# Kernel tuning notes

Hardware: AMD Instinct MI355X
Metric: run time of the kernel (lower is better)

Reference implementation:

```python
import jax, jax.numpy as jnp
import numpy as np

H = 128
N_ATOMS = 20000
N_BONDS = 60000
BATCH = 8


def _linear_params(key, fan_in, fan_out, bias=True):
    kw, kb = jax.random.split(key)
    lim = 1.0 / np.sqrt(fan_in)
    W = jax.random.uniform(kw, (fan_in, fan_out), jnp.float32, -lim, lim)
    if bias:
        b = jax.random.uniform(kb, (fan_out,), jnp.float32, -lim, lim)
        return W, b
    return W


def setup_inputs() -> dict:
    key = jax.random.key(0)
    ks = jax.random.split(key, 12)
    h = jax.random.normal(ks[0], (BATCH, N_ATOMS, H), jnp.float32)
    x = jax.random.normal(ks[1], (BATCH, N_ATOMS, 3), jnp.float32)
    bond_indices = jax.random.randint(ks[2], (N_BONDS, 2), 0, N_ATOMS, jnp.int64)
    Wm1, bm1 = _linear_params(ks[3], 2 * H + 1, H)
    Wm2, bm2 = _linear_params(ks[4], H, H)
    Wn1, bn1 = _linear_params(ks[5], 2 * H, H)
    Wn2, bn2 = _linear_params(ks[6], H, H)
    Wc1, bc1 = _linear_params(ks[7], H, H)
    # xavier_uniform gain=0.001 for final coord layer [1, H] in torch -> [H, 1] here
    lim = 0.001 * np.sqrt(6.0 / (H + 1))
    Wc2 = jax.random.uniform(ks[8], (H, 1), jnp.float32, -lim, lim)
    return dict(h=h, x=x, bond_indices=bond_indices,
                Wm1=Wm1, bm1=bm1, Wm2=Wm2, bm2=bm2,
                Wn1=Wn1, bn1=bn1, Wn2=Wn2, bn2=bn2,
                Wc1=Wc1, bc1=bc1, Wc2=Wc2)


def reference(h, x, bond_indices, Wm1, bm1, Wm2, bm2, Wn1, bn1, Wn2, bn2, Wc1, bc1, Wc2):
    silu = jax.nn.silu
    n_atoms = h.shape[1]
    src = bond_indices[:, 0]
    dst = bond_indices[:, 1]

    h_src = h[:, src, :]            # [B, E, H]
    h_dst = h[:, dst, :]
    coord_diff = x[:, dst, :] - x[:, src, :]   # [B, E, 3]
    dist = jnp.linalg.norm(coord_diff, axis=-1, keepdims=True)  # [B, E, 1]

    mi = jnp.concatenate([h_src, h_dst, dist], axis=-1)  # [B, E, 2H+1]
    messages = silu(silu(mi @ Wm1 + bm1) @ Wm2 + bm2)    # [B, E, H]

    aggregated = jnp.zeros_like(h).at[:, dst, :].add(messages).at[:, src, :].add(messages)

    h_in = jnp.concatenate([h, aggregated], axis=-1)     # [B, N, 2H]
    h_out = h + (silu(h_in @ Wn1 + bn1) @ Wn2 + bn2)

    coord_weights = silu(messages @ Wc1 + bc1) @ Wc2     # [B, E, 1]
    coord_diff_norm = coord_diff / (dist + 1e-8)
    upd = coord_diff_norm * coord_weights                # [B, E, 3]
    coord_update = jnp.zeros_like(x).at[:, dst, :].add(upd).at[:, src, :].add(-upd)

    ones = jnp.ones(src.shape[0], dtype=h.dtype)
    bond_counts = jnp.zeros(n_atoms, dtype=h.dtype).at[dst].add(ones).at[src].add(ones)
    bond_counts = jnp.clip(bond_counts, 1.0, None)
    x_out = x + coord_update / bond_counts[None, :, None]
    return h_out, x_out
```

## Files before the change

### kernel.cpp

```cpp
#include <hip/hip_runtime.h>


#define H      128
#define NA     20000
#define NB     60000
#define NBATCH 8
#define ADJ_CAP 32

typedef __bf16 bf16;
typedef __bf16 bf16x4 __attribute__((ext_vector_type(4)));
typedef __bf16 bf16x8 __attribute__((ext_vector_type(8)));
typedef float  f32x4  __attribute__((ext_vector_type(4)));

__device__ __forceinline__ float silu_f(float v) {
  float e = __expf(-v);
  return v * __builtin_amdgcn_rcpf(1.0f + e);
}

__device__ __forceinline__ int tswz(int row, int col) {
  return (row << 7) + (((((col) >> 3) ^ (row & 7)) << 3) | (col & 7));
}

__global__ void cast_h(const float* __restrict__ src, bf16* __restrict__ dst) {
  int i = blockIdx.x * 256 + threadIdx.x;
  float4 v = *(const float4*)(src + (size_t)i * 4);
  bf16x4 t = {(bf16)v.x, (bf16)v.y, (bf16)v.z, (bf16)v.w};
  *(bf16x4*)(dst + (size_t)i * 4) = t;
}

__global__ void pack_w(const float* __restrict__ src, bf16* __restrict__ dst,
                       int K) {
  int i = blockIdx.x * 256 + threadIdx.x;
  if (i >= K * 128) return;
  int k = i >> 7, n = i & 127;
  int nt = n >> 4, ks = k >> 5;
  int lane = (((k >> 3) & 3) << 4) | (n & 15);
  int j = k & 7;
  int KS = K >> 5;
  dst[((((nt * KS + ks) * 64) + lane) << 3) + j] = (bf16)src[i];
}

__global__ void build_adj2(const int* __restrict__ bonds,
                           int* __restrict__ degI, int* __restrict__ adj2) {
  int e = blockIdx.x * 256 + threadIdx.x;
  if (e >= NB) return;
  int s = bonds[2 * e], d = bonds[2 * e + 1];
  int p = atomicAdd(&degI[s], 1);
  if (p < ADJ_CAP) adj2[s * ADJ_CAP + p] = (e << 1);
  p = atomicAdd(&degI[d], 1);
  if (p < ADJ_CAP) adj2[d * ADJ_CAP + p] = (e << 1) | 1;
}

__global__ __launch_bounds__(256, 6) void msg_kernel(
    const bf16* __restrict__ hb, const float* __restrict__ x,
    const int* __restrict__ bonds,
    const bf16* __restrict__ W1p, const float* __restrict__ bm1,
    const bf16* __restrict__ W2p, const float* __restrict__ bm2,
    const float* __restrict__ w1c,
    const bf16* __restrict__ Wc1p, const float* __restrict__ bc1,
    const float* __restrict__ Wc2,
    bf16* __restrict__ msgOut, float* __restrict__ updv) {
  __shared__ __align__(16) bf16 Tbuf[32 * 128];
  __shared__ float cds[32 * 3];
  __shared__ float dists[32];
  __shared__ float bm1s[128], bm2s[128], w1cs[128], bc1s[128], wc2s[128];
  __shared__ float cwpart[2][32];

  const int tid = threadIdx.x, blk = blockIdx.x;

  if (tid < 32) {
    int Rg = blk * 32 + tid;
    int bond = Rg >> 3, batch = Rg & 7;
    int s = bonds[2 * bond], dn = bonds[2 * bond + 1];
    const float* xs = x + (size_t)(batch * NA + s) * 3;
    const float* xd = x + (size_t)(batch * NA + dn) * 3;
    float c0 = xd[0] - xs[0], c1 = xd[1] - xs[1], c2 = xd[2] - xs[2];
    cds[tid * 3 + 0] = c0; cds[tid * 3 + 1] = c1; cds[tid * 3 + 2] = c2;
    dists[tid] = sqrtf(c0 * c0 + c1 * c1 + c2 * c2);
  }
  if (tid < 128) {
    bm1s[tid] = bm1[tid]; bm2s[tid] = bm2[tid]; w1cs[tid] = w1c[tid];
    bc1s[tid] = bc1[tid]; wc2s[tid] = Wc2[tid];
  }
  __syncthreads();

  const int lane = tid & 63;
  const int quad = lane >> 4, l16 = lane & 15;
  const int wave = tid >> 6;
  const int rowBase = (wave >> 1) * 16;
  const int colG = wave & 1;
  const int colBase = colG * 64;
  const bf16x8* W1v = (const bf16x8*)W1p;
  const bf16x8* W2v = (const bf16x8*)W2p;
  const bf16x8* Wc1v = (const bf16x8*)Wc1p;

  const int RgA = blk * 32 + rowBase + l16;
  const int bondA = RgA >> 3, batA = RgA & 7;
  const bf16* hsrc = hb + (size_t)(batA * NA + bonds[2 * bondA]) * H;
  const bf16* hdst = hb + (size_t)(batA * NA + bonds[2 * bondA + 1]) * H;

  f32x4 acc[4];
#pragma unroll
  for (int nt = 0; nt < 4; nt++) acc[nt] = (f32x4){0.f, 0.f, 0.f, 0.f};

#pragma unroll
  for (int ks = 0; ks < 4; ks++) {
    bf16x8 a = *(const bf16x8*)(hsrc + ks * 32 + quad * 8);
#pragma unroll
    for (int nt = 0; nt < 4; nt++) {
      bf16x8 b = W1v[((colG * 4 + nt) * 8 + ks) * 64 + lane];
      acc[nt] = __builtin_amdgcn_mfma_f32_16x16x32_bf16(a, b, acc[nt], 0, 0, 0);
    }
  }
#pragma unroll
  for (int ks = 4; ks < 8; ks++) {
    bf16x8 a = *(const bf16x8*)(hdst + (ks - 4) * 32 + quad * 8);
#pragma unroll
    for (int nt = 0; nt < 4; nt++) {
      bf16x8 b = W1v[((colG * 4 + nt) * 8 + ks) * 64 + lane];
      acc[nt] = __builtin_amdgcn_mfma_f32_16x16x32_bf16(a, b, acc[nt], 0, 0, 0);
    }
  }
#pragma unroll
  for (int nt = 0; nt < 4; nt++) {
    int col = colBase + nt * 16 + l16;
    float bb = bm1s[col], wc = w1cs[col];
#pragma unroll
    for (int reg = 0; reg < 4; reg++) {
      int row = rowBase + quad * 4 + reg;
      float v = acc[nt][reg] + bb + dists[row] * wc;
      Tbuf[tswz(row, col)] = (bf16)silu_f(v);
    }
  }
  __syncthreads();

#pragma unroll
  for (int nt = 0; nt < 4; nt++) acc[nt] = (f32x4){0.f, 0.f, 0.f, 0.f};
#pragma unroll
  for (int ks = 0; ks < 4; ks++) {
    bf16x8 a = *(const bf16x8*)&Tbuf[tswz(rowBase + l16, ks * 32 + quad * 8)];
#pragma unroll
    for (int nt = 0; nt < 4; nt++) {
      bf16x8 b = W2v[((colG * 4 + nt) * 4 + ks) * 64 + lane];
      acc[nt] = __builtin_amdgcn_mfma_f32_16x16x32_bf16(a, b, acc[nt], 0, 0, 0);
    }
  }
  __syncthreads();
#pragma unroll
  for (int nt = 0; nt < 4; nt++) {
    int col = colBase + nt * 16 + l16;
    float bb = bm2s[col];
#pragma unroll
    for (int reg = 0; reg < 4; reg++) {
      int row = rowBase + quad * 4 + reg;
      Tbuf[tswz(row, col)] = (bf16)silu_f(acc[nt][reg] + bb);
    }
  }
  __syncthreads();

#pragma unroll
  for (int nt = 0; nt < 4; nt++) acc[nt] = (f32x4){0.f, 0.f, 0.f, 0.f};
#pragma unroll
  for (int ks = 0; ks < 4; ks++) {
    bf16x8 a = *(const bf16x8*)&Tbuf[tswz(rowBase + l16, ks * 32 + quad * 8)];
#pragma unroll
    for (int nt = 0; nt < 4; nt++) {
      bf16x8 b = Wc1v[((colG * 4 + nt) * 4 + ks) * 64 + lane];
      acc[nt] = __builtin_amdgcn_mfma_f32_16x16x32_bf16(a, b, acc[nt], 0, 0, 0);
    }
  }

#pragma unroll
  for (int i = 0; i < 2; i++) {
    int item = i * 64 + lane;
    int row = rowBase + (item >> 3);
    int cg = colG * 8 + (item & 7);
    *(bf16x8*)&msgOut[(size_t)(blk * 32 + row) * H + cg * 8] =
        *(const bf16x8*)&Tbuf[tswz(row, cg * 8)];
  }

  float cwp[4] = {0.f, 0.f, 0.f, 0.f};
#pragma unroll
  for (int nt = 0; nt < 4; nt++) {
    int col = colBase + nt * 16 + l16;
    float bb = bc1s[col], w2 = wc2s[col];
#pragma unroll
    for (int reg = 0; reg < 4; reg++)
      cwp[reg] += silu_f(acc[nt][reg] + bb) * w2;
  }
#pragma unroll
  for (int reg = 0; reg < 4; reg++) {
    float s = cwp[reg];
    s += __shfl_xor(s, 1);
    s += __shfl_xor(s, 2);
    s += __shfl_xor(s, 4);
    s += __shfl_xor(s, 8);
    cwp[reg] = s;
  }
  if (l16 == 0) {
#pragma unroll
    for (int reg = 0; reg < 4; reg++)
      cwpart[colG][rowBase + quad * 4 + reg] = cwp[reg];
  }
  __syncthreads();
  if (colG == 0 && l16 == 0) {
#pragma unroll
    for (int reg = 0; reg < 4; reg++) {
      int row = rowBase + quad * 4 + reg;
      size_t Rg = (size_t)blk * 32 + row;
      float cw = cwpart[0][row] + cwpart[1][row];
      float inv = 1.0f / (dists[row] + 1e-8f);
#pragma unroll
      for (int c = 0; c < 3; c++)
        updv[Rg * 3 + c] = cds[row * 3 + c] * inv * cw;
    }
  }
}

__global__ __launch_bounds__(256, 6) void node_kernel(
    const float* __restrict__ h, const bf16* __restrict__ hb,
    const bf16* __restrict__ msg, const float* __restrict__ updv,
    const int* __restrict__ degI, const int* __restrict__ adj2,
    const bf16* __restrict__ Wn1p, const float* __restrict__ bn1,
    const bf16* __restrict__ Wn2p, const float* __restrict__ bn2,
    const float* __restrict__ x,
    float* __restrict__ hout, float* __restrict__ xout) {
  __shared__ __align__(16) bf16 Abuf[32 * 128];
  __shared__ __align__(16) bf16 Tbuf[32 * 128];

  const int tid = threadIdx.x, blk = blockIdx.x;

  {
    const int row = tid >> 3, c8 = tid & 7;
    const int Rg = blk * 32 + row;
    const int atomA = Rg % NA, batA = Rg / NA;
    int deg = degI[atomA];
    if (deg > ADJ_CAP) deg = ADJ_CAP;
    const int* ap = adj2 + atomA * ADJ_CAP;
    float a16[16];
#pragma unroll
    for (int t = 0; t < 16; t++) a16[t] = 0.f;
    float sx = 0.f, sy = 0.f, sz = 0.f;
    int j = 0;
    for (; j + 4 <= deg; j += 4) {
      int4 e4 = *(const int4*)&ap[j];
      const bf16* m0 = msg + ((size_t)(e4.x >> 1) * 8 + batA) * H + c8 * 16;
      const bf16* m1 = msg + ((size_t)(e4.y >> 1) * 8 + batA) * H + c8 * 16;
      const bf16* m2 = msg + ((size_t)(e4.z >> 1) * 8 + batA) * H + c8 * 16;
      const bf16* m3 = msg + ((size_t)(e4.w >> 1) * 8 + batA) * H + c8 * 16;
      bf16x8 v0 = *(const bf16x8*)(m0), v1 = *(const bf16x8*)(m0 + 8);
      bf16x8 u0 = *(const bf16x8*)(m1), u1 = *(const bf16x8*)(m1 + 8);
      bf16x8 p0 = *(const bf16x8*)(m2), p1 = *(const bf16x8*)(m2 + 8);
      bf16x8 q0 = *(const bf16x8*)(m3), q1 = *(const bf16x8*)(m3 + 8);
      if (c8 == 0) {
        float sg0 = (e4.x & 1) ? 1.0f : -1.0f;
        float sg1 = (e4.y & 1) ? 1.0f : -1.0f;
        float sg2 = (e4.z & 1) ? 1.0f : -1.0f;
        float sg3 = (e4.w & 1) ? 1.0f : -1.0f;
        const float* uv0 = updv + ((size_t)(e4.x >> 1) * 8 + batA) * 3;
        const float* uv1 = updv + ((size_t)(e4.y >> 1) * 8 + batA) * 3;
        const float* uv2 = updv + ((size_t)(e4.z >> 1) * 8 + batA) * 3;
        const float* uv3 = updv + ((size_t)(e4.w >> 1) * 8 + batA) * 3;
        sx += sg0 * uv0[0] + sg1 * uv1[0] + sg2 * uv2[0] + sg3 * uv3[0];
        sy += sg0 * uv0[1] + sg1 * uv1[1] + sg2 * uv2[1] + sg3 * uv3[1];
        sz += sg0 * uv0[2] + sg1 * uv1[2] + sg2 * uv2[2] + sg3 * uv3[2];
      }
#pragma unroll
      for (int t = 0; t < 8; t++) {
        a16[t]     += ((float)v0[t] + (float)u0[t]) + ((float)p0[t] + (float)q0[t]);
        a16[8 + t] += ((float)v1[t] + (float)u1[t]) + ((float)p1[t] + (float)q1[t]);
      }
    }
    for (; j < deg; j++) {
      int ent0 = ap[j];
      const bf16* m0 = msg + ((size_t)(ent0 >> 1) * 8 + batA) * H + c8 * 16;
      bf16x8 v0 = *(const bf16x8*)(m0);
      bf16x8 v1 = *(const bf16x8*)(m0 + 8);
      if (c8 == 0) {
        float sg0 = (ent0 & 1) ? 1.0f : -1.0f;
        const float* uv0 = updv + ((size_t)(ent0 >> 1) * 8 + batA) * 3;
        sx += sg0 * uv0[0]; sy += sg0 * uv0[1]; sz += sg0 * uv0[2];
      }
#pragma unroll
      for (int t = 0; t < 8; t++) {
        a16[t]     += (float)v0[t];
        a16[8 + t] += (float)v1[t];
      }
    }
    if (c8 == 0) {
      float cnt = deg < 1 ? 1.0f : (float)deg;
      float inv = 1.0f / cnt;
      size_t o = (size_t)Rg * 3;
      xout[o + 0] = x[o + 0] + sx * inv;
      xout[o + 1] = x[o + 1] + sy * inv;
      xout[o + 2] = x[o + 2] + sz * inv;
    }
    bf16x8 w0, w1;
#pragma unroll
    for (int t = 0; t < 8; t++) { w0[t] = (bf16)a16[t]; w1[t] = (bf16)a16[8 + t]; }
    *(bf16x8*)&Abuf[tswz(row, c8 * 16)]     = w0;
    *(bf16x8*)&Abuf[tswz(row, c8 * 16 + 8)] = w1;
  }
  __syncthreads();

  const int lane = tid & 63, wave = tid >> 6;
  const int quad = lane >> 4, l16 = lane & 15;
  const int rowG = (wave >> 1) * 16, colG = wave & 1, colBase = colG * 64;
  const int RgA = blk * 32 + rowG + l16;
  const bf16* hrow = hb + (size_t)RgA * H;
  const bf16x8* W1v = (const bf16x8*)Wn1p;
  const bf16x8* W2v = (const bf16x8*)Wn2p;

  f32x4 acc[4];
#pragma unroll
  for (int nt = 0; nt < 4; nt++) acc[nt] = (f32x4){0.f, 0.f, 0.f, 0.f};

#pragma unroll
  for (int ks = 0; ks < 4; ks++) {
    bf16x8 a = *(const bf16x8*)(hrow + ks * 32 + quad * 8);
#pragma unroll
    for (int nt = 0; nt < 4; nt++) {
      bf16x8 b = W1v[((colG * 4 + nt) * 8 + ks) * 64 + lane];
      acc[nt] = __builtin_amdgcn_mfma_f32_16x16x32_bf16(a, b, acc[nt], 0, 0, 0);
    }
  }
#pragma unroll
  for (int ks2 = 0; ks2 < 4; ks2++) {
    bf16x8 a = *(const bf16x8*)&Abuf[tswz(rowG + l16, ks2 * 32 + quad * 8)];
#pragma unroll
    for (int nt = 0; nt < 4; nt++) {
      bf16x8 b = W1v[((colG * 4 + nt) * 8 + 4 + ks2) * 64 + lane];
      acc[nt] = __builtin_amdgcn_mfma_f32_16x16x32_bf16(a, b, acc[nt], 0, 0, 0);
    }
  }
#pragma unroll
  for (int nt = 0; nt < 4; nt++) {
    int col = colBase + nt * 16 + l16;
    float bb = bn1[col];
#pragma unroll
    for (int reg = 0; reg < 4; reg++) {
      int row = rowG + quad * 4 + reg;
      Tbuf[tswz(row, col)] = (bf16)silu_f(acc[nt][reg] + bb);
    }
  }
  __syncthreads();

#pragma unroll
  for (int nt = 0; nt < 4; nt++) acc[nt] = (f32x4){0.f, 0.f, 0.f, 0.f};
#pragma unroll
  for (int ks = 0; ks < 4; ks++) {
    bf16x8 a = *(const bf16x8*)&Tbuf[tswz(rowG + l16, ks * 32 + quad * 8)];
#pragma unroll
    for (int nt = 0; nt < 4; nt++) {
      bf16x8 b = W2v[((colG * 4 + nt) * 4 + ks) * 64 + lane];
      acc[nt] = __builtin_amdgcn_mfma_f32_16x16x32_bf16(a, b, acc[nt], 0, 0, 0);
    }
  }
#pragma unroll
  for (int nt = 0; nt < 4; nt++) {
    int col = colBase + nt * 16 + l16;
    float bb = bn2[col];
#pragma unroll
    for (int reg = 0; reg < 4; reg++) {
      size_t Ro = (size_t)blk * 32 + rowG + quad * 4 + reg;
      hout[Ro * H + col] = h[Ro * H + col] + acc[nt][reg] + bb;
    }
  }
}

extern "C" void kernel_launch(void* const* d_in, const int* in_sizes, int n_in,
                              void* d_out, int out_size, void* d_ws,
                              size_t ws_size, hipStream_t stream) {
  const float* h    = (const float*)d_in[0];
  const float* x    = (const float*)d_in[1];
  const int*  bonds = (const int*)d_in[2];
  const float* Wm1  = (const float*)d_in[3];
  const float* bm1  = (const float*)d_in[4];
  const float* Wm2  = (const float*)d_in[5];
  const float* bm2  = (const float*)d_in[6];
  const float* Wn1  = (const float*)d_in[7];
  const float* bn1  = (const float*)d_in[8];
  const float* Wn2  = (const float*)d_in[9];
  const float* bn2  = (const float*)d_in[10];
  const float* Wc1  = (const float*)d_in[11];
  const float* bc1  = (const float*)d_in[12];
  const float* Wc2  = (const float*)d_in[13];

  float* out  = (float*)d_out;
  float* hout = out;
  float* xout = out + (size_t)NBATCH * NA * H;

  char* ws = (char*)d_ws;
  const size_t OFF_DEG  = 0;
  const size_t OFF_W1   = 163840;
  const size_t OFF_W2   = OFF_W1 + 65536;
  const size_t OFF_WN1  = OFF_W2 + 32768;
  const size_t OFF_WN2  = OFF_WN1 + 65536;
  const size_t OFF_WC1  = OFF_WN2 + 32768;
  const size_t OFF_ADJ2 = 393216;
  const size_t OFF_UPDV = 2953216;
  const size_t OFF_HB   = 8713216;
  const size_t OFF_MSG  = 49673216;

  int*   degI = (int*)(ws + OFF_DEG);
  bf16*  W1p  = (bf16*)(ws + OFF_W1);
  bf16*  W2p  = (bf16*)(ws + OFF_W2);
  bf16*  Wn1p = (bf16*)(ws + OFF_WN1);
  bf16*  Wn2p = (bf16*)(ws + OFF_WN2);
  bf16*  Wc1p = (bf16*)(ws + OFF_WC1);
  int*   adj2 = (int*)(ws + OFF_ADJ2);
  float* updv = (float*)(ws + OFF_UPDV);
  bf16*  hb   = (bf16*)(ws + OFF_HB);
  bf16*  msgB = (bf16*)(ws + OFF_MSG);

  (void)hipMemsetAsync(degI, 0, NA * sizeof(int), stream);

  cast_h<<<NBATCH * NA * H / 1024, 256, 0, stream>>>(h, hb);
  pack_w<<<128, 256, 0, stream>>>(Wm1, W1p, 256);
  pack_w<<<64, 256, 0, stream>>>(Wm2, W2p, 128);
  pack_w<<<128, 256, 0, stream>>>(Wn1, Wn1p, 256);
  pack_w<<<64, 256, 0, stream>>>(Wn2, Wn2p, 128);
  pack_w<<<64, 256, 0, stream>>>(Wc1, Wc1p, 128);

  build_adj2<<<(NB + 255) / 256, 256, 0, stream>>>(bonds, degI, adj2);

  msg_kernel<<<NB * NBATCH / 32, 256, 0, stream>>>(
      hb, x, bonds, W1p, bm1, W2p, bm2, Wm1 + 256 * H, Wc1p, bc1, Wc2,
      msgB, updv);
  node_kernel<<<NBATCH * NA / 32, 256, 0, stream>>>(
      h, hb, msgB, updv, degI, adj2, Wn1p, bn1, Wn2p, bn2, x,
      hout, xout);
}
```

Baseline: 509.9 us.

## Double msg_kernel rows per block and prefetch adjacency with null-padded entries

msg_kernel now handles 64 rows per block instead of 32. Each wave computes two 16-row MFMA tiles that share the same weight fragment loads, which halves weight traffic per row and gives more independent MFMAs to overlap. The occupancy hint drops from 6 to 4 blocks per SIMD to make room for the extra registers. Separately, the adjacency list is pre-filled with a null entry that points to a zeroed msg/updv slot. This lets node_kernel load the first eight neighbours unconditionally and start the gathers before reading the degree, at the cost of wasted gathers for low-degree atoms and an extra init kernel.

New measurement: 503.2 us. No clear change (-1.3%).

```diff
diff --git a/kernel.cpp b/kernel.cpp
--- a/kernel.cpp
+++ b/kernel.cpp
@@ -6,6 +6,7 @@
 #define NB     60000
 #define NBATCH 8
 #define ADJ_CAP 32
+#define NULL_ENT (NB << 1)
 
 typedef __bf16 bf16;
 typedef __bf16 bf16x4 __attribute__((ext_vector_type(4)));
@@ -40,6 +41,12 @@
   dst[((((nt * KS + ks) * 64) + lane) << 3) + j] = (bf16)src[i];
 }
 
+__global__ void init_adj(int* __restrict__ degI, int* __restrict__ adj2) {
+  int i = blockIdx.x * 256 + threadIdx.x;
+  if (i < NA) degI[i] = 0;
+  if (i < NA * ADJ_CAP) adj2[i] = NULL_ENT;
+}
+
 __global__ void build_adj2(const int* __restrict__ bonds,
                            int* __restrict__ degI, int* __restrict__ adj2) {
   int e = blockIdx.x * 256 + threadIdx.x;
@@ -51,7 +58,7 @@
   if (p < ADJ_CAP) adj2[d * ADJ_CAP + p] = (e << 1) | 1;
 }
 
-__global__ __launch_bounds__(256, 6) void msg_kernel(
+__global__ __launch_bounds__(256, 4) void msg_kernel(
     const bf16* __restrict__ hb, const float* __restrict__ x,
     const int* __restrict__ bonds,
     const bf16* __restrict__ W1p, const float* __restrict__ bm1,
@@ -60,16 +67,16 @@
     const bf16* __restrict__ Wc1p, const float* __restrict__ bc1,
     const float* __restrict__ Wc2,
     bf16* __restrict__ msgOut, float* __restrict__ updv) {
-  __shared__ __align__(16) bf16 Tbuf[32 * 128];
-  __shared__ float cds[32 * 3];
-  __shared__ float dists[32];
+  __shared__ __align__(16) bf16 Tbuf[64 * 128];
+  __shared__ float cds[64 * 3];
+  __shared__ float dists[64];
   __shared__ float bm1s[128], bm2s[128], w1cs[128], bc1s[128], wc2s[128];
-  __shared__ float cwpart[2][32];
+  __shared__ float cwpart[2][64];
 
   const int tid = threadIdx.x, blk = blockIdx.x;
 
-  if (tid < 32) {
-    int Rg = blk * 32 + tid;
+  if (tid < 64) {
+    int Rg = blk * 64 + tid;
     int bond = Rg >> 3, batch = Rg & 7;
     int s = bonds[2 * bond], dn = bonds[2 * bond + 1];
     const float* xs = x + (size_t)(batch * NA + s) * 3;
@@ -87,38 +94,49 @@
   const int lane = tid & 63;
   const int quad = lane >> 4, l16 = lane & 15;
   const int wave = tid >> 6;
-  const int rowBase = (wave >> 1) * 16;
+  const int rowBase = (wave >> 1) * 32;
   const int colG = wave & 1;
   const int colBase = colG * 64;
   const bf16x8* W1v = (const bf16x8*)W1p;
   const bf16x8* W2v = (const bf16x8*)W2p;
   const bf16x8* Wc1v = (const bf16x8*)Wc1p;
 
-  const int RgA = blk * 32 + rowBase + l16;
-  const int bondA = RgA >> 3, batA = RgA & 7;
-  const bf16* hsrc = hb + (size_t)(batA * NA + bonds[2 * bondA]) * H;
-  const bf16* hdst = hb + (size_t)(batA * NA + bonds[2 * bondA + 1]) * H;
-
-  f32x4 acc[4];
-#pragma unroll
-  for (int nt = 0; nt < 4; nt++) acc[nt] = (f32x4){0.f, 0.f, 0.f, 0.f};
+  const int Rg0 = blk * 64 + rowBase + l16;
+  const int bn0 = Rg0 >> 3, bat0 = Rg0 & 7;
+  const bf16* hs0 = hb + (size_t)(bat0 * NA + bonds[2 * bn0]) * H;
+  const bf16* hd0 = hb + (size_t)(bat0 * NA + bonds[2 * bn0 + 1]) * H;
+  const int Rg1 = Rg0 + 16;
+  const int bn1_ = Rg1 >> 3, bat1 = Rg1 & 7;
+  const bf16* hs1 = hb + (size_t)(bat1 * NA + bonds[2 * bn1_]) * H;
+  const bf16* hd1 = hb + (size_t)(bat1 * NA + bonds[2 * bn1_ + 1]) * H;
+
+  f32x4 acc0[4], acc1[4];
+#pragma unroll
+  for (int nt = 0; nt < 4; nt++) {
+    acc0[nt] = (f32x4){0.f, 0.f, 0.f, 0.f};
+    acc1[nt] = (f32x4){0.f, 0.f, 0.f, 0.f};
+  }
 
 #pragma unroll
   for (int ks = 0; ks < 4; ks++) {
-    bf16x8 a = *(const bf16x8*)(hsrc + ks * 32 + quad * 8);
+    bf16x8 a0 = *(const bf16x8*)(hs0 + ks * 32 + quad * 8);
+    bf16x8 a1 = *(const bf16x8*)(hs1 + ks * 32 + quad * 8);
 #pragma unroll
     for (int nt = 0; nt < 4; nt++) {
       bf16x8 b = W1v[((colG * 4 + nt) * 8 + ks) * 64 + lane];
-      acc[nt] = __builtin_amdgcn_mfma_f32_16x16x32_bf16(a, b, acc[nt], 0, 0, 0);
+      acc0[nt] = __builtin_amdgcn_mfma_f32_16x16x32_bf16(a0, b, acc0[nt], 0, 0, 0);
+      acc1[nt] = __builtin_amdgcn_mfma_f32_16x16x32_bf16(a1, b, acc1[nt], 0, 0, 0);
     }
   }
 #pragma unroll
   for (int ks = 4; ks < 8; ks++) {
-    bf16x8 a = *(const bf16x8*)(hdst + (ks - 4) * 32 + quad * 8);
+    bf16x8 a0 = *(const bf16x8*)(hd0 + (ks - 4) * 32 + quad * 8);
+    bf16x8 a1 = *(const bf16x8*)(hd1 + (ks - 4) * 32 + quad * 8);
 #pragma unroll
     for (int nt = 0; nt < 4; nt++) {
       bf16x8 b = W1v[((colG * 4 + nt) * 8 + ks) * 64 + lane];
-      acc[nt] = __builtin_amdgcn_mfma_f32_16x16x32_bf16(a, b, acc[nt], 0, 0, 0);
+      acc0[nt] = __builtin_amdgcn_mfma_f32_16x16x32_bf16(a0, b, acc0[nt], 0, 0, 0);
+      acc1[nt] = __builtin_amdgcn_mfma_f32_16x16x32_bf16(a1, b, acc1[nt], 0, 0, 0);
     }
   }
 #pragma unroll
@@ -127,22 +145,28 @@
     float bb = bm1s[col], wc = w1cs[col];
 #pragma unroll
     for (int reg = 0; reg < 4; reg++) {
-      int row = rowBase + quad * 4 + reg;
-      float v = acc[nt][reg] + bb + dists[row] * wc;
-      Tbuf[tswz(row, col)] = (bf16)silu_f(v);
-    }
-  }
-  __syncthreads();
-
-#pragma unroll
-  for (int nt = 0; nt < 4; nt++) acc[nt] = (f32x4){0.f, 0.f, 0.f, 0.f};
+      int row0 = rowBase + quad * 4 + reg;
+      int row1 = row0 + 16;
+      Tbuf[tswz(row0, col)] = (bf16)silu_f(acc0[nt][reg] + bb + dists[row0] * wc);
+      Tbuf[tswz(row1, col)] = (bf16)silu_f(acc1[nt][reg] + bb + dists[row1] * wc);
+    }
+  }
+  __syncthreads();
+
+#pragma unroll
+  for (int nt = 0; nt < 4; nt++) {
+    acc0[nt] = (f32x4){0.f, 0.f, 0.f, 0.f};
+    acc1[nt] = (f32x4){0.f, 0.f, 0.f, 0.f};
+  }
 #pragma unroll
   for (int ks = 0; ks < 4; ks++) {
-    bf16x8 a = *(const bf16x8*)&Tbuf[tswz(rowBase + l16, ks * 32 + quad * 8)];
+    bf16x8 a0 = *(const bf16x8*)&Tbuf[tswz(rowBase + l16, ks * 32 + quad * 8)];
+    bf16x8 a1 = *(const bf16x8*)&Tbuf[tswz(rowBase + 16 + l16, ks * 32 + quad * 8)];
 #pragma unroll
     for (int nt = 0; nt < 4; nt++) {
       bf16x8 b = W2v[((colG * 4 + nt) * 4 + ks) * 64 + lane];
-      acc[nt] = __builtin_amdgcn_mfma_f32_16x16x32_bf16(a, b, acc[nt], 0, 0, 0);
+      acc0[nt] = __builtin_amdgcn_mfma_f32_16x16x32_bf16(a0, b, acc0[nt], 0, 0, 0);
+      acc1[nt] = __builtin_amdgcn_mfma_f32_16x16x32_bf16(a1, b, acc1[nt], 0, 0, 0);
     }
   }
   __syncthreads();
@@ -152,67 +176,82 @@
     float bb = bm2s[col];
 #pragma unroll
     for (int reg = 0; reg < 4; reg++) {
-      int row = rowBase + quad * 4 + reg;
-      Tbuf[tswz(row, col)] = (bf16)silu_f(acc[nt][reg] + bb);
-    }
-  }
-  __syncthreads();
-
-#pragma unroll
-  for (int nt = 0; nt < 4; nt++) acc[nt] = (f32x4){0.f, 0.f, 0.f, 0.f};
+      int row0 = rowBase + quad * 4 + reg;
+      int row1 = row0 + 16;
+      Tbuf[tswz(row0, col)] = (bf16)silu_f(acc0[nt][reg] + bb);
+      Tbuf[tswz(row1, col)] = (bf16)silu_f(acc1[nt][reg] + bb);
+    }
+  }
+  __syncthreads();
+
+#pragma unroll
+  for (int nt = 0; nt < 4; nt++) {
+    acc0[nt] = (f32x4){0.f, 0.f, 0.f, 0.f};
+    acc1[nt] = (f32x4){0.f, 0.f, 0.f, 0.f};
+  }
 #pragma unroll
   for (int ks = 0; ks < 4; ks++) {
-    bf16x8 a = *(const bf16x8*)&Tbuf[tswz(rowBase + l16, ks * 32 + quad * 8)];
+    bf16x8 a0 = *(const bf16x8*)&Tbuf[tswz(rowBase + l16, ks * 32 + quad * 8)];
+    bf16x8 a1 = *(const bf16x8*)&Tbuf[tswz(rowBase + 16 + l16, ks * 32 + quad * 8)];
 #pragma unroll
     for (int nt = 0; nt < 4; nt++) {
       bf16x8 b = Wc1v[((colG * 4 + nt) * 4 + ks) * 64 + lane];
-      acc[nt] = __builtin_amdgcn_mfma_f32_16x16x32_bf16(a, b, acc[nt], 0, 0, 0);
-    }
-  }
-
-#pragma unroll
-  for (int i = 0; i < 2; i++) {
-    int item = i * 64 + lane;
-    int row = rowBase + (item >> 3);
-    int cg = colG * 8 + (item & 7);
-    *(bf16x8*)&msgOut[(size_t)(blk * 32 + row) * H + cg * 8] =
+      acc0[nt] = __builtin_amdgcn_mfma_f32_16x16x32_bf16(a0, b, acc0[nt], 0, 0, 0);
+      acc1[nt] = __builtin_amdgcn_mfma_f32_16x16x32_bf16(a1, b, acc1[nt], 0, 0, 0);
+    }
+  }
+
+#pragma unroll
+  for (int i = 0; i < 4; i++) {
+    int item = i * 256 + tid;
+    int row = item >> 4, cg = item & 15;
+    *(bf16x8*)&msgOut[(size_t)(blk * 64 + row) * H + cg * 8] =
         *(const bf16x8*)&Tbuf[tswz(row, cg * 8)];
   }
 
-  float cwp[4] = {0.f, 0.f, 0.f, 0.f};
+  float cwp0[4] = {0.f, 0.f, 0.f, 0.f};
+  float cwp1[4] = {0.f, 0.f, 0.f, 0.f};
 #pragma unroll
   for (int nt = 0; nt < 4; nt++) {
     int col = colBase + nt * 16 + l16;
     float bb = bc1s[col], w2 = wc2s[col];
 #pragma unroll
-    for (int reg = 0; reg < 4; reg++)
-      cwp[reg] += silu_f(acc[nt][reg] + bb) * w2;
+    for (int reg = 0; reg < 4; reg++) {
+      cwp0[reg] += silu_f(acc0[nt][reg] + bb) * w2;
+      cwp1[reg] += silu_f(acc1[nt][reg] + bb) * w2;
+    }
   }
 #pragma unroll
   for (int reg = 0; reg < 4; reg++) {
-    float s = cwp[reg];
-    s += __shfl_xor(s, 1);
-    s += __shfl_xor(s, 2);
-    s += __shfl_xor(s, 4);
-    s += __shfl_xor(s, 8);
-    cwp[reg] = s;
+    float s0 = cwp0[reg], s1 = cwp1[reg];
+    s0 += __shfl_xor(s0, 1); s1 += __shfl_xor(s1, 1);
+    s0 += __shfl_xor(s0, 2); s1 += __shfl_xor(s1, 2);
+    s0 += __shfl_xor(s0, 4); s1 += __shfl_xor(s1, 4);
+    s0 += __shfl_xor(s0, 8); s1 += __shfl_xor(s1, 8);
+    cwp0[reg] = s0; cwp1[reg] = s1;
   }
   if (l16 == 0) {
 #pragma unroll
-    for (int reg = 0; reg < 4; reg++)
-      cwpart[colG][rowBase + quad * 4 + reg] = cwp[reg];
+    for (int reg = 0; reg < 4; reg++) {
+      int row0 = rowBase + quad * 4 + reg;
+      cwpart[colG][row0] = cwp0[reg];
+      cwpart[colG][row0 + 16] = cwp1[reg];
+    }
   }
   __syncthreads();
   if (colG == 0 && l16 == 0) {
 #pragma unroll
     for (int reg = 0; reg < 4; reg++) {
-      int row = rowBase + quad * 4 + reg;
-      size_t Rg = (size_t)blk * 32 + row;
-      float cw = cwpart[0][row] + cwpart[1][row];
-      float inv = 1.0f / (dists[row] + 1e-8f);
-#pragma unroll
-      for (int c = 0; c < 3; c++)
-        updv[Rg * 3 + c] = cds[row * 3 + c] * inv * cw;
+#pragma unroll
+      for (int rs = 0; rs < 2; rs++) {
+        int row = rowBase + quad * 4 + reg + rs * 16;
+        size_t Rg = (size_t)blk * 64 + row;
+        float cw = cwpart[0][row] + cwpart[1][row];
+        float inv = 1.0f / (dists[row] + 1e-8f);
+#pragma unroll
+        for (int c = 0; c < 3; c++)
+          updv[Rg * 3 + c] = cds[row * 3 + c] * inv * cw;
+      }
     }
   }
 }
@@ -234,16 +273,18 @@
     const int row = tid >> 3, c8 = tid & 7;
     const int Rg = blk * 32 + row;
     const int atomA = Rg % NA, batA = Rg / NA;
+    const int* ap = adj2 + atomA * ADJ_CAP;
     int deg = degI[atomA];
+    int4 eA = *(const int4*)&ap[0];
+    int4 eB = *(const int4*)&ap[4];
     if (deg > ADJ_CAP) deg = ADJ_CAP;
-    const int* ap = adj2 + atomA * ADJ_CAP;
+
     float a16[16];
 #pragma unroll
     for (int t = 0; t < 16; t++) a16[t] = 0.f;
     float sx = 0.f, sy = 0.f, sz = 0.f;
-    int j = 0;
-    for (; j + 4 <= deg; j += 4) {
-      int4 e4 = *(const int4*)&ap[j];
+
+    auto gather4 = [&](int4 e4) {
       const bf16* m0 = msg + ((size_t)(e4.x >> 1) * 8 + batA) * H + c8 * 16;
       const bf16* m1 = msg + ((size_t)(e4.y >> 1) * 8 + batA) * H + c8 * 16;
       const bf16* m2 = msg + ((size_t)(e4.z >> 1) * 8 + batA) * H + c8 * 16;
@@ -270,7 +311,12 @@
         a16[t]     += ((float)v0[t] + (float)u0[t]) + ((float)p0[t] + (float)q0[t]);
         a16[8 + t] += ((float)v1[t] + (float)u1[t]) + ((float)p1[t] + (float)q1[t]);
       }
-    }
+    };
+
+    gather4(eA);
+    gather4(eB);
+    int j = 8;
+    for (; j + 4 <= deg; j += 4) gather4(*(const int4*)&ap[j]);
     for (; j < deg; j++) {
       int ent0 = ap[j];
       const bf16* m0 = msg + ((size_t)(ent0 >> 1) * 8 + batA) * H + c8 * 16;
@@ -399,8 +445,8 @@
   const size_t OFF_WC1  = OFF_WN2 + 32768;
   const size_t OFF_ADJ2 = 393216;
   const size_t OFF_UPDV = 2953216;
-  const size_t OFF_HB   = 8713216;
-  const size_t OFF_MSG  = 49673216;
+  const size_t OFF_HB   = 8717312;
+  const size_t OFF_MSG  = 49677312;
 
   int*   degI = (int*)(ws + OFF_DEG);
   bf16*  W1p  = (bf16*)(ws + OFF_W1);
@@ -413,7 +459,10 @@
   bf16*  hb   = (bf16*)(ws + OFF_HB);
   bf16*  msgB = (bf16*)(ws + OFF_MSG);
 
-  (void)hipMemsetAsync(degI, 0, NA * sizeof(int), stream);
+  (void)hipMemsetAsync(msgB + (size_t)NB * 8 * H, 0, 8 * H * sizeof(bf16),
+                       stream);
+  (void)hipMemsetAsync(updv + (size_t)NB * 8 * 3, 0, 8 * 3 * sizeof(float),
+                       stream);
 
   cast_h<<<NBATCH * NA * H / 1024, 256, 0, stream>>>(h, hb);
   pack_w<<<128, 256, 0, stream>>>(Wm1, W1p, 256);
@@ -422,9 +471,10 @@
   pack_w<<<64, 256, 0, stream>>>(Wn2, Wn2p, 128);
   pack_w<<<64, 256, 0, stream>>>(Wc1, Wc1p, 128);
 
+  init_adj<<<(NA * ADJ_CAP + 255) / 256, 256, 0, stream>>>(degI, adj2);
   build_adj2<<<(NB + 255) / 256, 256, 0, stream>>>(bonds, degI, adj2);
 
-  msg_kernel<<<NB * NBATCH / 32, 256, 0, stream>>>(
+  msg_kernel<<<NB * NBATCH / 64, 256, 0, stream>>>(
       hb, x, bonds, W1p, bm1, W2p, bm2, Wm1 + 256 * H, Wc1p, bc1, Wc2,
       msgB, updv);
   node_kernel<<<NBATCH * NA / 32, 256, 0, stream>>>(
```
